# Optimization experiments

Measured on AMD Instinct MI355X. Metric: run time of the kernel, lower is better.

The kernel has to match this reference:

```python
import jax, jax.numpy as jnp
import numpy as np
from jax import lax

B, T, D = 8, 2048, 1024


def setup_inputs() -> dict:
    key = jax.random.key(0)
    ks = jax.random.split(key, 8)
    s = 1.0 / np.sqrt(D)
    x = jax.random.normal(ks[0], (B, T, D), dtype=jnp.float32)
    Wq = jax.random.uniform(ks[1], (D, D), jnp.float32, -s, s)
    bq = jax.random.uniform(ks[2], (D,), jnp.float32, -s, s)
    Wk = jax.random.uniform(ks[3], (D, D), jnp.float32, -s, s)
    bk = jax.random.uniform(ks[4], (D,), jnp.float32, -s, s)
    Wv = jax.random.uniform(ks[5], (D, D), jnp.float32, -s, s)
    bv = jax.random.uniform(ks[6], (D,), jnp.float32, -s, s)
    decay = jnp.full((D,), 0.9, dtype=jnp.float32)  # nn.Parameter(ones*0.9)
    return {"x": x, "Wq": Wq, "bq": bq, "Wk": Wk, "bk": bk,
            "Wv": Wv, "bv": bv, "decay": decay}


def reference(x, Wq, bq, Wk, bk, Wv, bv, decay):
    # projections (torch Linear: x @ W.T + b)
    q = jnp.einsum('btd,ed->bte', x, Wq) + bq
    k = jnp.einsum('btd,ed->bte', x, Wk) + bk
    v = jnp.einsum('btd,ed->bte', x, Wv) + bv
    kv = k * v  # [B,T,D]

    # diagonal-decay linear recurrence: mem_t = decay * mem_{t-1} + kv_t
    def step(mem, kv_t):
        mem = decay * mem + kv_t  # [B,D]
        return mem, mem

    mem0 = jnp.zeros((B, D), dtype=x.dtype)
    _, mems = lax.scan(step, mem0, jnp.swapaxes(kv, 0, 1))  # mems: [T,B,D]
    out = q * jnp.swapaxes(mems, 0, 1)  # output_t = q_t * mem_t
    return out
```

## Files before the change

### kernel.cpp

```cpp
#include <hip/hip_runtime.h>
#include <cstdint>

typedef unsigned short ushort_t;
typedef __bf16 bf16x8 __attribute__((ext_vector_type(8)));
typedef float f32x4 __attribute__((ext_vector_type(4)));

#define B_ 8
#define T_ 2048
#define D_ 1024
#define M_ (B_ * T_)
#define NCHUNK 32
#define CHUNKLEN 64

__device__ __forceinline__ ushort_t f2bf(float f) {
    union { float f; uint32_t u; } v; v.f = f;
    uint32_t u = v.u;
    uint32_t r = (u + 0x7fffu + ((u >> 16) & 1u)) >> 16;
    return (ushort_t)r;
}
__device__ __forceinline__ float bf2f(ushort_t h) {
    union { uint32_t u; float f; } v; v.u = ((uint32_t)h) << 16;
    return v.f;
}

__device__ __forceinline__ void async16(const ushort_t* g, ushort_t* l) {
    __builtin_amdgcn_global_load_lds(
        (const __attribute__((address_space(1))) void*)g,
        (__attribute__((address_space(3))) void*)l, 16, 0, 0);
}

__global__ __launch_bounds__(256) void cast_bf16(const float* __restrict__ src,
                                                 ushort_t* __restrict__ dst, int n4) {
    int i = blockIdx.x * blockDim.x + threadIdx.x;
    if (i < n4) {
        float4 v = ((const float4*)src)[i];
        ushort4 o;
        o.x = f2bf(v.x); o.y = f2bf(v.y); o.z = f2bf(v.z); o.w = f2bf(v.w);
        ((ushort4*)dst)[i] = o;
    }
}

__global__ __launch_bounds__(256) void qkv_gemm(
    const ushort_t* __restrict__ xb, const ushort_t* __restrict__ Wb,
    const float* __restrict__ bq, const float* __restrict__ bk,
    const float* __restrict__ bv,
    float* __restrict__ qout, ushort_t* __restrict__ kbf, ushort_t* __restrict__ vbf) {
    __shared__ ushort_t As[128 * 32];
    __shared__ ushort_t Bs[128 * 32];

    const int mb = blockIdx.x, nb = blockIdx.y;
    const int w = nb >> 3;
    const int m0 = mb * 128, n0 = (nb & 7) * 128;
    const ushort_t* Wsrc = Wb + (size_t)w * D_ * D_;

    const int t = threadIdx.x;
    const int lane = t & 63, wv = t >> 6;
    const int wr = (wv >> 1) * 64, wc = (wv & 1) * 64;

    f32x4 acc[4][4];
#pragma unroll
    for (int i = 0; i < 4; ++i)
#pragma unroll
        for (int j = 0; j < 4; ++j) acc[i][j] = (f32x4){0.f, 0.f, 0.f, 0.f};

    const int r0 = t >> 2, r1 = (t + 256) >> 2;
    const int c0 = (t & 3) * 8;

    const int ka = (lane >> 4) * 8;
    const int rowa = wr + (lane & 15);
    const int rowb = wc + (lane & 15);

    for (int kt = 0; kt < 32; ++kt) {
        const int k0 = kt * 32;
        async16(xb + (size_t)(m0 + r0) * D_ + k0 + c0, &As[t * 8]);
        async16(xb + (size_t)(m0 + r1) * D_ + k0 + c0, &As[(t + 256) * 8]);
        async16(Wsrc + (size_t)(n0 + r0) * D_ + k0 + c0, &Bs[t * 8]);
        async16(Wsrc + (size_t)(n0 + r1) * D_ + k0 + c0, &Bs[(t + 256) * 8]);
        __syncthreads();

        bf16x8 af[4], bfr[4];
#pragma unroll
        for (int i = 0; i < 4; ++i)
            af[i] = *(const bf16x8*)&As[(rowa + i * 16) * 32 + ka];
#pragma unroll
        for (int j = 0; j < 4; ++j)
            bfr[j] = *(const bf16x8*)&Bs[(rowb + j * 16) * 32 + ka];
#pragma unroll
        for (int i = 0; i < 4; ++i)
#pragma unroll
            for (int j = 0; j < 4; ++j)
                acc[i][j] = __builtin_amdgcn_mfma_f32_16x16x32_bf16(
                    af[i], bfr[j], acc[i][j], 0, 0, 0);
        __syncthreads();
    }

    const float* bias = (w == 0) ? bq : ((w == 1) ? bk : bv);
    const int colq = lane & 15;
    const int rowq = (lane >> 4) * 4;
#pragma unroll
    for (int i = 0; i < 4; ++i) {
#pragma unroll
        for (int j = 0; j < 4; ++j) {
            const int cg = n0 + wc + j * 16 + colq;
            const float bval = bias[cg];
#pragma unroll
            for (int r = 0; r < 4; ++r) {
                const int rg = m0 + wr + i * 16 + rowq + r;
                const float val = acc[i][j][r] + bval;
                const size_t off = (size_t)rg * D_ + cg;
                if (w == 0)      qout[off] = val;
                else if (w == 1) kbf[off] = f2bf(val);
                else             vbf[off] = f2bf(val);
            }
        }
    }
}

__global__ __launch_bounds__(1024) void scan_chunks(
    const ushort_t* __restrict__ kb, const ushort_t* __restrict__ vb,
    const float* __restrict__ decay, float* __restrict__ S) {
    const int b = blockIdx.x >> 5, c = blockIdx.x & 31;
    const int d = threadIdx.x;
    const float dec = decay[d];
    float m = 0.f;
    size_t base = ((size_t)b * T_ + c * CHUNKLEN) * D_ + d;
#pragma unroll 8
    for (int i = 0; i < CHUNKLEN; ++i) {
        const size_t o = base + (size_t)i * D_;
        m = fmaf(dec, m, bf2f(kb[o]) * bf2f(vb[o]));
    }
    S[((size_t)b * NCHUNK + c) * D_ + d] = m;
}

__global__ __launch_bounds__(256) void scan_carry(
    const float* __restrict__ S, const float* __restrict__ decay,
    float* __restrict__ P) {
    const int idx = blockIdx.x * blockDim.x + threadIdx.x;
    const int d = idx & (D_ - 1), b = idx >> 10;
    const float dec = decay[d];
    float dL = dec;
    dL *= dL; dL *= dL; dL *= dL; dL *= dL; dL *= dL; dL *= dL;
    float p = 0.f;
    for (int c = 0; c < NCHUNK; ++c) {
        const size_t o = ((size_t)b * NCHUNK + c) * D_ + d;
        P[o] = p;
        p = fmaf(dL, p, S[o]);
    }
}

__global__ __launch_bounds__(1024) void scan_final(
    const ushort_t* __restrict__ kb, const ushort_t* __restrict__ vb,
    const float* __restrict__ decay, const float* __restrict__ P,
    float* __restrict__ out) {
    const int b = blockIdx.x >> 5, c = blockIdx.x & 31;
    const int d = threadIdx.x;
    const float dec = decay[d];
    float m = P[((size_t)b * NCHUNK + c) * D_ + d];
    size_t base = ((size_t)b * T_ + c * CHUNKLEN) * D_ + d;
#pragma unroll 8
    for (int i = 0; i < CHUNKLEN; ++i) {
        const size_t o = base + (size_t)i * D_;
        m = fmaf(dec, m, bf2f(kb[o]) * bf2f(vb[o]));
        out[o] = out[o] * m;
    }
}

extern "C" void kernel_launch(void* const* d_in, const int* in_sizes, int n_in,
                              void* d_out, int out_size, void* d_ws, size_t ws_size,
                              hipStream_t stream) {
    const float* x     = (const float*)d_in[0];
    const float* Wq    = (const float*)d_in[1];
    const float* bq    = (const float*)d_in[2];
    const float* Wk    = (const float*)d_in[3];
    const float* bk    = (const float*)d_in[4];
    const float* Wv    = (const float*)d_in[5];
    const float* bv    = (const float*)d_in[6];
    const float* decay = (const float*)d_in[7];
    float* out = (float*)d_out;

    char* ws = (char*)d_ws;
    ushort_t* xb  = (ushort_t*)(ws);
    ushort_t* Wb  = (ushort_t*)(ws + 33554432);
    ushort_t* kbf = (ushort_t*)(ws + 39845888);
    ushort_t* vbf = (ushort_t*)(ws + 73400320);
    float*    S   = (float*)(ws + 106954752);
    float*    P   = (float*)(ws + 108003328);

    cast_bf16<<<(M_ * D_ / 4 + 255) / 256, 256, 0, stream>>>(x, xb, M_ * D_ / 4);
    cast_bf16<<<(D_ * D_ / 4 + 255) / 256, 256, 0, stream>>>(Wq, Wb, D_ * D_ / 4);
    cast_bf16<<<(D_ * D_ / 4 + 255) / 256, 256, 0, stream>>>(Wk, Wb + D_ * D_, D_ * D_ / 4);
    cast_bf16<<<(D_ * D_ / 4 + 255) / 256, 256, 0, stream>>>(Wv, Wb + 2 * D_ * D_, D_ * D_ / 4);

    dim3 g(M_ / 128, 24);
    qkv_gemm<<<g, 256, 0, stream>>>(xb, Wb, bq, bk, bv, out, kbf, vbf);

    scan_chunks<<<B_ * NCHUNK, 1024, 0, stream>>>(kbf, vbf, decay, S);
    scan_carry<<<(B_ * D_) / 256, 256, 0, stream>>>(S, decay, P);
    scan_final<<<B_ * NCHUNK, 1024, 0, stream>>>(kbf, vbf, decay, P, out);
}
```

Before: 304.2 us.

## Fuse k*v into GEMM epilogue, store q as bf16, swizzle LDS, retune scan

Splits the QKV GEMM into a Q GEMM and a fused K/V GEMM that computes k*v in its epilogue and writes a single bf16 kv tensor. This removes the separate k and v round trips through memory. q is now stored as bf16 instead of fp32, which halves its traffic but adds rounding error. The change also adds an XOR swizzle to the LDS tile layout to cut bank conflicts, merges the three weight casts into one launch, and changes the scan to 64 chunks of 32 with 2-wide vectorised accesses and smaller blocks. S and P now reuse the start of the xb workspace region, which is safe only because the scans run after the GEMMs.

```diff
diff --git a/kernel.cpp b/kernel.cpp
--- a/kernel.cpp
+++ b/kernel.cpp
@@ -9,8 +9,8 @@
 #define T_ 2048
 #define D_ 1024
 #define M_ (B_ * T_)
-#define NCHUNK 32
-#define CHUNKLEN 64
+#define NCHUNK 64
+#define CHUNKLEN 32
 
 __device__ __forceinline__ ushort_t f2bf(float f) {
     union { float f; uint32_t u; } v; v.f = f;
@@ -40,19 +40,27 @@
     }
 }
 
-__global__ __launch_bounds__(256) void qkv_gemm(
-    const ushort_t* __restrict__ xb, const ushort_t* __restrict__ Wb,
-    const float* __restrict__ bq, const float* __restrict__ bk,
-    const float* __restrict__ bv,
-    float* __restrict__ qout, ushort_t* __restrict__ kbf, ushort_t* __restrict__ vbf) {
+__global__ __launch_bounds__(256) void cast_w3(const float* __restrict__ wq,
+                                               const float* __restrict__ wk,
+                                               const float* __restrict__ wv,
+                                               ushort_t* __restrict__ dst) {
+    const int n4 = D_ * D_ / 4;
+    int i = blockIdx.x * blockDim.x + threadIdx.x;
+    const float* src = (i < n4) ? wq : ((i < 2 * n4) ? wk : wv);
+    int li = (i < n4) ? i : ((i < 2 * n4) ? i - n4 : i - 2 * n4);
+    float4 v = ((const float4*)src)[li];
+    ushort4 o;
+    o.x = f2bf(v.x); o.y = f2bf(v.y); o.z = f2bf(v.z); o.w = f2bf(v.w);
+    ((ushort4*)(dst))[i] = o;
+}
+
+__global__ __launch_bounds__(256) void gemm_q(
+    const ushort_t* __restrict__ xb, const ushort_t* __restrict__ Wq,
+    const float* __restrict__ bq, ushort_t* __restrict__ qb) {
     __shared__ ushort_t As[128 * 32];
     __shared__ ushort_t Bs[128 * 32];
 
-    const int mb = blockIdx.x, nb = blockIdx.y;
-    const int w = nb >> 3;
-    const int m0 = mb * 128, n0 = (nb & 7) * 128;
-    const ushort_t* Wsrc = Wb + (size_t)w * D_ * D_;
-
+    const int m0 = blockIdx.x * 128, n0 = blockIdx.y * 128;
     const int t = threadIdx.x;
     const int lane = t & 63, wv = t >> 6;
     const int wr = (wv >> 1) * 64, wc = (wv & 1) * 64;
@@ -63,28 +71,29 @@
 #pragma unroll
         for (int j = 0; j < 4; ++j) acc[i][j] = (f32x4){0.f, 0.f, 0.f, 0.f};
 
-    const int r0 = t >> 2, r1 = (t + 256) >> 2;
-    const int c0 = (t & 3) * 8;
-
-    const int ka = (lane >> 4) * 8;
+    const int r0 = t >> 2, r1 = r0 + 64;
+    const int sc = ((t & 3) ^ ((r0 >> 1) & 3)) * 8;
+
+    const int swq = ((lane & 15) >> 1) & 3;
+    const int csel = (((lane >> 4) ^ swq)) * 8;
     const int rowa = wr + (lane & 15);
     const int rowb = wc + (lane & 15);
 
     for (int kt = 0; kt < 32; ++kt) {
         const int k0 = kt * 32;
-        async16(xb + (size_t)(m0 + r0) * D_ + k0 + c0, &As[t * 8]);
-        async16(xb + (size_t)(m0 + r1) * D_ + k0 + c0, &As[(t + 256) * 8]);
-        async16(Wsrc + (size_t)(n0 + r0) * D_ + k0 + c0, &Bs[t * 8]);
-        async16(Wsrc + (size_t)(n0 + r1) * D_ + k0 + c0, &Bs[(t + 256) * 8]);
+        async16(xb + (size_t)(m0 + r0) * D_ + k0 + sc, &As[t * 8]);
+        async16(xb + (size_t)(m0 + r1) * D_ + k0 + sc, &As[(t + 256) * 8]);
+        async16(Wq + (size_t)(n0 + r0) * D_ + k0 + sc, &Bs[t * 8]);
+        async16(Wq + (size_t)(n0 + r1) * D_ + k0 + sc, &Bs[(t + 256) * 8]);
         __syncthreads();
 
         bf16x8 af[4], bfr[4];
 #pragma unroll
         for (int i = 0; i < 4; ++i)
-            af[i] = *(const bf16x8*)&As[(rowa + i * 16) * 32 + ka];
+            af[i] = *(const bf16x8*)&As[(rowa + i * 16) * 32 + csel];
 #pragma unroll
         for (int j = 0; j < 4; ++j)
-            bfr[j] = *(const bf16x8*)&Bs[(rowb + j * 16) * 32 + ka];
+            bfr[j] = *(const bf16x8*)&Bs[(rowb + j * 16) * 32 + csel];
 #pragma unroll
         for (int i = 0; i < 4; ++i)
 #pragma unroll
@@ -94,7 +103,6 @@
         __syncthreads();
     }
 
-    const float* bias = (w == 0) ? bq : ((w == 1) ? bk : bv);
     const int colq = lane & 15;
     const int rowq = (lane >> 4) * 4;
 #pragma unroll
@@ -102,34 +110,114 @@
 #pragma unroll
         for (int j = 0; j < 4; ++j) {
             const int cg = n0 + wc + j * 16 + colq;
-            const float bval = bias[cg];
+            const float bval = bq[cg];
 #pragma unroll
             for (int r = 0; r < 4; ++r) {
                 const int rg = m0 + wr + i * 16 + rowq + r;
-                const float val = acc[i][j][r] + bval;
-                const size_t off = (size_t)rg * D_ + cg;
-                if (w == 0)      qout[off] = val;
-                else if (w == 1) kbf[off] = f2bf(val);
-                else             vbf[off] = f2bf(val);
+                qb[(size_t)rg * D_ + cg] = f2bf(acc[i][j][r] + bval);
             }
         }
     }
 }
 
-__global__ __launch_bounds__(1024) void scan_chunks(
-    const ushort_t* __restrict__ kb, const ushort_t* __restrict__ vb,
-    const float* __restrict__ decay, float* __restrict__ S) {
-    const int b = blockIdx.x >> 5, c = blockIdx.x & 31;
-    const int d = threadIdx.x;
-    const float dec = decay[d];
-    float m = 0.f;
-    size_t base = ((size_t)b * T_ + c * CHUNKLEN) * D_ + d;
+__global__ __launch_bounds__(256, 2) void gemm_kv(
+    const ushort_t* __restrict__ xb, const ushort_t* __restrict__ Wk,
+    const ushort_t* __restrict__ Wv, const float* __restrict__ bk,
+    const float* __restrict__ bv, ushort_t* __restrict__ kvb) {
+    __shared__ ushort_t As[128 * 32];
+    __shared__ ushort_t Bk[128 * 32];
+    __shared__ ushort_t Bv[128 * 32];
+
+    const int m0 = blockIdx.x * 128, n0 = blockIdx.y * 128;
+    const int t = threadIdx.x;
+    const int lane = t & 63, wv = t >> 6;
+    const int wr = (wv >> 1) * 64, wc = (wv & 1) * 64;
+
+    f32x4 acck[4][4], accv[4][4];
+#pragma unroll
+    for (int i = 0; i < 4; ++i)
+#pragma unroll
+        for (int j = 0; j < 4; ++j) {
+            acck[i][j] = (f32x4){0.f, 0.f, 0.f, 0.f};
+            accv[i][j] = (f32x4){0.f, 0.f, 0.f, 0.f};
+        }
+
+    const int r0 = t >> 2, r1 = r0 + 64;
+    const int sc = ((t & 3) ^ ((r0 >> 1) & 3)) * 8;
+
+    const int swq = ((lane & 15) >> 1) & 3;
+    const int csel = (((lane >> 4) ^ swq)) * 8;
+    const int rowa = wr + (lane & 15);
+    const int rowb = wc + (lane & 15);
+
+    for (int kt = 0; kt < 32; ++kt) {
+        const int k0 = kt * 32;
+        async16(xb + (size_t)(m0 + r0) * D_ + k0 + sc, &As[t * 8]);
+        async16(xb + (size_t)(m0 + r1) * D_ + k0 + sc, &As[(t + 256) * 8]);
+        async16(Wk + (size_t)(n0 + r0) * D_ + k0 + sc, &Bk[t * 8]);
+        async16(Wk + (size_t)(n0 + r1) * D_ + k0 + sc, &Bk[(t + 256) * 8]);
+        async16(Wv + (size_t)(n0 + r0) * D_ + k0 + sc, &Bv[t * 8]);
+        async16(Wv + (size_t)(n0 + r1) * D_ + k0 + sc, &Bv[(t + 256) * 8]);
+        __syncthreads();
+
+        bf16x8 af[4], bk8[4], bv8[4];
+#pragma unroll
+        for (int i = 0; i < 4; ++i)
+            af[i] = *(const bf16x8*)&As[(rowa + i * 16) * 32 + csel];
+#pragma unroll
+        for (int j = 0; j < 4; ++j) {
+            bk8[j] = *(const bf16x8*)&Bk[(rowb + j * 16) * 32 + csel];
+            bv8[j] = *(const bf16x8*)&Bv[(rowb + j * 16) * 32 + csel];
+        }
+#pragma unroll
+        for (int i = 0; i < 4; ++i)
+#pragma unroll
+            for (int j = 0; j < 4; ++j) {
+                acck[i][j] = __builtin_amdgcn_mfma_f32_16x16x32_bf16(
+                    af[i], bk8[j], acck[i][j], 0, 0, 0);
+                accv[i][j] = __builtin_amdgcn_mfma_f32_16x16x32_bf16(
+                    af[i], bv8[j], accv[i][j], 0, 0, 0);
+            }
+        __syncthreads();
+    }
+
+    const int colq = lane & 15;
+    const int rowq = (lane >> 4) * 4;
+#pragma unroll
+    for (int i = 0; i < 4; ++i) {
+#pragma unroll
+        for (int j = 0; j < 4; ++j) {
+            const int cg = n0 + wc + j * 16 + colq;
+            const float bkv = bk[cg], bvv = bv[cg];
+#pragma unroll
+            for (int r = 0; r < 4; ++r) {
+                const int rg = m0 + wr + i * 16 + rowq + r;
+                const float kf = acck[i][j][r] + bkv;
+                const float vf = accv[i][j][r] + bvv;
+                kvb[(size_t)rg * D_ + cg] = f2bf(kf * vf);
+            }
+        }
+    }
+}
+
+__global__ __launch_bounds__(256) void scan_chunks(
+    const ushort_t* __restrict__ kvb, const float* __restrict__ decay,
+    float* __restrict__ S) {
+    const int b = blockIdx.x >> 7;
+    const int c = (blockIdx.x >> 1) & 63;
+    const int dg = blockIdx.x & 1;
+    const int d0 = dg * 512 + threadIdx.x * 2;
+    const float dc0 = decay[d0], dc1 = decay[d0 + 1];
+    float m0 = 0.f, m1 = 0.f;
+    size_t base = ((size_t)b * T_ + c * CHUNKLEN) * D_ + d0;
 #pragma unroll 8
     for (int i = 0; i < CHUNKLEN; ++i) {
-        const size_t o = base + (size_t)i * D_;
-        m = fmaf(dec, m, bf2f(kb[o]) * bf2f(vb[o]));
-    }
-    S[((size_t)b * NCHUNK + c) * D_ + d] = m;
+        ushort2 kv = *(const ushort2*)&kvb[base + (size_t)i * D_];
+        m0 = fmaf(dc0, m0, bf2f(kv.x));
+        m1 = fmaf(dc1, m1, bf2f(kv.y));
+    }
+    float2* so = (float2*)&S[((size_t)b * NCHUNK + c) * D_ + d0];
+    *so = make_float2(m0, m1);
 }
 
 __global__ __launch_bounds__(256) void scan_carry(
@@ -139,7 +227,7 @@
     const int d = idx & (D_ - 1), b = idx >> 10;
     const float dec = decay[d];
     float dL = dec;
-    dL *= dL; dL *= dL; dL *= dL; dL *= dL; dL *= dL; dL *= dL;
+    dL *= dL; dL *= dL; dL *= dL; dL *= dL; dL *= dL;
     float p = 0.f;
     for (int c = 0; c < NCHUNK; ++c) {
         const size_t o = ((size_t)b * NCHUNK + c) * D_ + d;
@@ -148,20 +236,26 @@
     }
 }
 
-__global__ __launch_bounds__(1024) void scan_final(
-    const ushort_t* __restrict__ kb, const ushort_t* __restrict__ vb,
+__global__ __launch_bounds__(256) void scan_final(
+    const ushort_t* __restrict__ kvb, const ushort_t* __restrict__ qb,
     const float* __restrict__ decay, const float* __restrict__ P,
     float* __restrict__ out) {
-    const int b = blockIdx.x >> 5, c = blockIdx.x & 31;
-    const int d = threadIdx.x;
-    const float dec = decay[d];
-    float m = P[((size_t)b * NCHUNK + c) * D_ + d];
-    size_t base = ((size_t)b * T_ + c * CHUNKLEN) * D_ + d;
+    const int b = blockIdx.x >> 7;
+    const int c = (blockIdx.x >> 1) & 63;
+    const int dg = blockIdx.x & 1;
+    const int d0 = dg * 512 + threadIdx.x * 2;
+    const float dc0 = decay[d0], dc1 = decay[d0 + 1];
+    const float2 p2 = *(const float2*)&P[((size_t)b * NCHUNK + c) * D_ + d0];
+    float m0 = p2.x, m1 = p2.y;
+    size_t base = ((size_t)b * T_ + c * CHUNKLEN) * D_ + d0;
 #pragma unroll 8
     for (int i = 0; i < CHUNKLEN; ++i) {
         const size_t o = base + (size_t)i * D_;
-        m = fmaf(dec, m, bf2f(kb[o]) * bf2f(vb[o]));
-        out[o] = out[o] * m;
+        ushort2 kv = *(const ushort2*)&kvb[o];
+        ushort2 q2 = *(const ushort2*)&qb[o];
+        m0 = fmaf(dc0, m0, bf2f(kv.x));
+        m1 = fmaf(dc1, m1, bf2f(kv.y));
+        *(float2*)&out[o] = make_float2(bf2f(q2.x) * m0, bf2f(q2.y) * m1);
     }
 }
 
@@ -181,20 +275,22 @@
     char* ws = (char*)d_ws;
     ushort_t* xb  = (ushort_t*)(ws);
     ushort_t* Wb  = (ushort_t*)(ws + 33554432);
-    ushort_t* kbf = (ushort_t*)(ws + 39845888);
-    ushort_t* vbf = (ushort_t*)(ws + 73400320);
-    float*    S   = (float*)(ws + 106954752);
-    float*    P   = (float*)(ws + 108003328);
+    ushort_t* qb  = (ushort_t*)(ws + 39845888);
+    ushort_t* kvb = (ushort_t*)(ws + 73400320);
+    float*    S   = (float*)(ws);
+    float*    P   = (float*)(ws + 2097152);
+
+    ushort_t* Wkb = Wb + D_ * D_;
+    ushort_t* Wvb = Wb + 2 * D_ * D_;
 
     cast_bf16<<<(M_ * D_ / 4 + 255) / 256, 256, 0, stream>>>(x, xb, M_ * D_ / 4);
-    cast_bf16<<<(D_ * D_ / 4 + 255) / 256, 256, 0, stream>>>(Wq, Wb, D_ * D_ / 4);
-    cast_bf16<<<(D_ * D_ / 4 + 255) / 256, 256, 0, stream>>>(Wk, Wb + D_ * D_, D_ * D_ / 4);
-    cast_bf16<<<(D_ * D_ / 4 + 255) / 256, 256, 0, stream>>>(Wv, Wb + 2 * D_ * D_, D_ * D_ / 4);
-
-    dim3 g(M_ / 128, 24);
-    qkv_gemm<<<g, 256, 0, stream>>>(xb, Wb, bq, bk, bv, out, kbf, vbf);
-
-    scan_chunks<<<B_ * NCHUNK, 1024, 0, stream>>>(kbf, vbf, decay, S);
+    cast_w3<<<(3 * D_ * D_ / 4) / 256, 256, 0, stream>>>(Wq, Wk, Wv, Wb);
+
+    dim3 g(M_ / 128, 8);
+    gemm_q<<<g, 256, 0, stream>>>(xb, Wb, bq, qb);
+    gemm_kv<<<g, 256, 0, stream>>>(xb, Wkb, Wvb, bk, bv, kvb);
+
+    scan_chunks<<<B_ * NCHUNK * 2, 256, 0, stream>>>(kvb, decay, S);
     scan_carry<<<(B_ * D_) / 256, 256, 0, stream>>>(S, decay, P);
-    scan_final<<<B_ * NCHUNK, 1024, 0, stream>>>(kbf, vbf, decay, P, out);
-}
+    scan_final<<<B_ * NCHUNK * 2, 256, 0, stream>>>(kvb, qb, decay, P, out);
+}
```

Result: faster. 289.6 us (-4.8%).
